# Kernel tuning notes

Hardware: AMD Instinct MI355X
Metric: run time of the kernel (lower is better)

Reference implementation:

```python
import jax, jax.numpy as jnp
import numpy as np

VOCAB = 256
EMB = 128
HID = 512
OUT = 256
B = 64
L = 1024


def setup_inputs() -> dict:
    key = jax.random.key(0)
    ks = jax.random.split(key, 6)
    x = jax.random.randint(ks[0], (B, L), 0, VOCAB, dtype=jnp.int32)
    hidden = jnp.zeros((B, HID), dtype=jnp.float32)
    embedding = jax.random.normal(ks[1], (VOCAB, EMB), dtype=jnp.float32)
    W_e = jax.random.normal(ks[2], (EMB, HID), dtype=jnp.float32) * 0.01
    W_h = jax.random.normal(ks[3], (HID, HID), dtype=jnp.float32) * 0.01
    b_h = jnp.zeros((1, HID), dtype=jnp.float32)
    W_o = jax.random.normal(ks[4], (HID, OUT), dtype=jnp.float32) * 0.01
    b_o = jnp.zeros((OUT,), dtype=jnp.float32)
    return {"x": x, "hidden": hidden, "embedding": embedding, "W_e": W_e,
            "W_h": W_h, "b_h": b_h, "W_o": W_o, "b_o": b_o}


def reference(x, hidden, embedding, W_e, W_h, b_h, W_o, b_o):
    # x: [b, l] int ids -> embed: [l, b, emb] (time-major for the scan)
    x_embed = embedding[x]                      # [b, l, emb]
    x_embed = jnp.swapaxes(x_embed, 0, 1)       # [l, b, emb]
    # Precompute input projection for all timesteps (same math, batched):
    hx_all = jnp.einsum('lbe,eh->lbh', x_embed, W_e)  # [l, b, hid]

    def step(h_prev, hx_t):
        h_t = jnp.tanh(hx_t + h_prev @ W_h + b_h)
        return h_t, h_t

    final_hidden, outputs = jax.lax.scan(step, hidden, hx_all)  # outputs: [l, b, hid]
    outputs = jnp.swapaxes(outputs, 0, 1)                        # [b, l, hid]
    logits = outputs @ W_o + b_o                                  # [b, l, out]
    return logits, final_hidden
```

## Files before the change

kernel.cpp:

```cpp
#include <hip/hip_runtime.h>

typedef float f32x4 __attribute__((ext_vector_type(4)));
typedef int   i32x4 __attribute__((ext_vector_type(4)));
typedef short s16x8 __attribute__((ext_vector_type(8)));

#define VOCAB 256
#define EMB   128
#define HID   512
#define OUT_D 256
#define BATCH 64
#define SEQ   1024

__device__ __forceinline__ unsigned short f2bf(float f) {
  unsigned u = __builtin_bit_cast(unsigned, f);
  u += 0x7fffu + ((u >> 16) & 1u);
  return (unsigned short)(u >> 16);
}

__global__ void k_e2(const float* __restrict__ emb, const float* __restrict__ We,
                     const float* __restrict__ bh, float* __restrict__ E2)
{
  __shared__ float el[EMB];
  const int v = blockIdx.x, c = threadIdx.x;
  if (c < EMB) el[c] = emb[v * EMB + c];
  __syncthreads();
  float s = bh[c];
  #pragma unroll
  for (int e = 0; e < EMB; ++e) s += el[e] * We[e * HID + c];
  E2[v * HID + c] = s;
}

__global__ void k_whfrag(const float* __restrict__ Wh, i32x4* __restrict__ WhF)
{
  const int g = blockIdx.x * 256 + threadIdx.x;
  const int lane = g & 63, frag = g >> 6;
  const int kt = frag & 7, nt = (frag >> 3) & 3, w = frag >> 5;
  const int col = (w << 6) + (nt << 4) + (lane & 15);
  const int kb  = (kt << 6) + ((lane >> 4) << 4);
  int wd[4];
  #pragma unroll
  for (int q = 0; q < 4; ++q) {
    int b[4];
    #pragma unroll
    for (int j = 0; j < 4; ++j) {
      float s = Wh[(kb + q * 4 + j) * HID + col] * 2048.f;
      s = fminf(fmaxf(s, -127.f), 127.f);
      b[j] = __float2int_rn(s) & 255;
    }
    wd[q] = b[0] | (b[1] << 8) | (b[2] << 16) | (b[3] << 24);
  }
  i32x4 v = {wd[0], wd[1], wd[2], wd[3]};
  WhF[g] = v;
}

__global__ void k_wot(const float* __restrict__ Wo, unsigned short* __restrict__ WoT)
{
  const int k = blockIdx.x;
  const int c = threadIdx.x;
  WoT[c * HID + k] = f2bf(Wo[k * OUT_D + c] * (1.0f / 127.0f));
}

__global__ __launch_bounds__(512, 2) void k_scan(
    const int* __restrict__ x, const float* __restrict__ h0,
    const float* __restrict__ E2, const i32x4* __restrict__ WhF,
    char* __restrict__ hist, float* __restrict__ fh)
{
  __shared__ __align__(16) char hbuf[2][HID];
  const int tid  = threadIdx.x;
  const int wv   = tid >> 6, lane = tid & 63;
  const int lrow = lane & 15, lhi = lane >> 4;
  const int row  = blockIdx.x;
  const int col  = (wv << 6) + (lhi << 4) + lrow;

  i32x4 bfr[4][8];
  #pragma unroll
  for (int nt = 0; nt < 4; ++nt)
    #pragma unroll
    for (int kt = 0; kt < 8; ++kt)
      bfr[nt][kt] = WhF[((((wv << 2) + nt) << 3) + kt) * 64 + lane];

  {
    float s = fminf(fmaxf(h0[(row << 9) + tid] * 127.f, -127.f), 127.f);
    hbuf[0][tid] = (char)__float2int_rn(s);
  }

  const int id0 = x[(row << 10) + 0];
  int idA = x[(row << 10) + 1], idB;
  float hxA = E2[(id0 << 9) + col], hxB;
  __syncthreads();

  const float inv = 1.f / (127.f * 2048.f);
  const float TC  = 2.8853900817779268f;

#define STEP(T, PH, HXU, HXP, IDU, IDL)                                       \
  {                                                                           \
    const int t_ = (T);                                                       \
           \
    i32x4 fv;                                                                 \
    if (tid < 32) fv = *(const i32x4*)(&hbuf[PH][tid << 4]);                  \
                 \
    HXP = E2[((IDU) << 9) + col];                                             \
                                               \
    IDL = x[(row << 10) + ((t_ + 2 > SEQ - 1) ? SEQ - 1 : t_ + 2)];           \
      \
    i32x4 acc[4] = {};                                                        \
    _Pragma("unroll") for (int kt = 0; kt < 8; ++kt) {                        \
      i32x4 a = *(const i32x4*)(&hbuf[PH][(kt << 6) + (lhi << 4)]);           \
      _Pragma("unroll") for (int nt = 0; nt < 4; ++nt)                        \
        acc[nt] = __builtin_amdgcn_mfma_i32_16x16x64_i8(a, bfr[nt][kt],       \
                                                        acc[nt], 0, 0, 0);    \
    }                                                                         \
                     \
    if (t_ > 0 && tid < 32)                                                   \
      __builtin_nontemporal_store(fv, (i32x4*)(hist +                         \
          (((size_t)(row << 10) + (t_ - 1)) << 10) + (tid << 4)));            \
      \
    int a01 = (lhi & 1) ? acc[1][0] : acc[0][0];                              \
    int a23 = (lhi & 1) ? acc[3][0] : acc[2][0];                              \
    int av  = (lhi & 2) ? a23 : a01;                                          \
                              \
    float z = fmaf((float)av, inv, HXU);                                      \
    float e = __builtin_amdgcn_exp2f(z * TC);                                 \
    float h = fmaf(-2.f, __builtin_amdgcn_rcpf(1.f + e), 1.f);                \
    hbuf[1 - (PH)][col] = (char)__float2int_rn(h * 127.f);                    \
    if (t_ == SEQ - 1) fh[(row << 9) + col] = h;                              \
    asm volatile("s_waitcnt lgkmcnt(0)" ::: "memory");                        \
    __builtin_amdgcn_sched_barrier(0);                                        \
    __builtin_amdgcn_s_barrier();                                             \
    __builtin_amdgcn_sched_barrier(0);                                        \
  }

  for (int T2 = 0; T2 < SEQ / 2; ++T2) {
    STEP(2 * T2,     0, hxA, hxB, idA, idB)
    STEP(2 * T2 + 1, 1, hxB, hxA, idB, idA)
  }
#undef STEP

  if (tid < 32) {
    i32x4 fv = *(const i32x4*)(&hbuf[0][tid << 4]);
    __builtin_nontemporal_store(fv, (i32x4*)(hist +
        (((size_t)(row << 10) + (SEQ - 1)) << 10) + (tid << 4)));
  }
}

__global__ __launch_bounds__(256) void k_logits(const char* __restrict__ hist,
                                                const unsigned short* __restrict__ WoT,
                                                const float* __restrict__ bo, float* out)
{
  __shared__ __align__(16) char As[64 * 1024];
  const int tid = threadIdx.x;
  const int m0 = blockIdx.x * 64;

  for (int i = tid; i < 1024; i += 256) {
    const int row = i >> 4, seg = i & 15;
    const char* src = hist + (size_t)(m0 + row) * 1024 + seg * 32;
    i32x4 w0 = *(const i32x4*)(src);
    i32x4 w1 = *(const i32x4*)(src + 16);
    unsigned od[16];
    #pragma unroll
    for (int d = 0; d < 8; ++d) {
      const unsigned dw = (unsigned)(d < 4 ? w0[d] : w1[d - 4]);
      const int q0 = (int)(signed char)(dw & 0xffu);
      const int q1 = (int)(signed char)((dw >> 8) & 0xffu);
      const int q2 = (int)(signed char)((dw >> 16) & 0xffu);
      const int q3 = (int)(signed char)(dw >> 24);
      const unsigned u0 = __builtin_bit_cast(unsigned, (float)q0);
      const unsigned u1 = __builtin_bit_cast(unsigned, (float)q1);
      const unsigned u2 = __builtin_bit_cast(unsigned, (float)q2);
      const unsigned u3 = __builtin_bit_cast(unsigned, (float)q3);
      od[2 * d]     = (u0 >> 16) | (u1 & 0xffff0000u);
      od[2 * d + 1] = (u2 >> 16) | (u3 & 0xffff0000u);
    }
    #pragma unroll
    for (int q = 0; q < 4; ++q) {
      i32x4 v = {(int)od[4 * q], (int)od[4 * q + 1],
                 (int)od[4 * q + 2], (int)od[4 * q + 3]};
      const int off = seg * 64 + q * 16;
      *(i32x4*)(&As[row * 1024 + (off ^ ((row & 7) << 4))]) = v;
    }
  }
  __syncthreads();

  const int wv = tid >> 6, lane = tid & 63, lrow = lane & 15, lhi = lane >> 4;
  const int cb = wv << 6;
  f32x4 acc[4][4] = {};
  #pragma unroll
  for (int kt = 0; kt < 16; ++kt) {
    s16x8 a[4], b[4];
    #pragma unroll
    for (int mt = 0; mt < 4; ++mt) {
      const int row = mt * 16 + lrow;
      a[mt] = *(const s16x8*)(&As[row * 1024 + ((kt * 64 + lhi * 16) ^ ((row & 7) << 4))]);
    }
    #pragma unroll
    for (int nt = 0; nt < 4; ++nt) {
      const int col = cb + nt * 16 + lrow;
      b[nt] = *(const s16x8*)((const char*)WoT + col * 1024 + kt * 64 + lhi * 16);
    }
    #pragma unroll
    for (int mt = 0; mt < 4; ++mt)
      #pragma unroll
      for (int nt = 0; nt < 4; ++nt)
        acc[mt][nt] = __builtin_amdgcn_mfma_f32_16x16x32_bf16(a[mt], b[nt], acc[mt][nt], 0, 0, 0);
  }
  #pragma unroll
  for (int nt = 0; nt < 4; ++nt) {
    const float bb = bo[cb + nt * 16 + lrow];
    #pragma unroll
    for (int mt = 0; mt < 4; ++mt)
      #pragma unroll
      for (int r = 0; r < 4; ++r)
        out[(size_t)(m0 + mt * 16 + lhi * 4 + r) * OUT_D + cb + nt * 16 + lrow] =
            acc[mt][nt][r] + bb;
  }
}

extern "C" void kernel_launch(void* const* d_in, const int* in_sizes, int n_in,
                              void* d_out, int out_size, void* d_ws, size_t ws_size,
                              hipStream_t stream)
{
  const int*   x   = (const int*)  d_in[0];
  const float* h0  = (const float*)d_in[1];
  const float* emb = (const float*)d_in[2];
  const float* We  = (const float*)d_in[3];
  const float* Wh  = (const float*)d_in[4];
  const float* bh  = (const float*)d_in[5];
  const float* Wo  = (const float*)d_in[6];
  const float* bo  = (const float*)d_in[7];
  float* out = (float*)d_out;
  char*  ws  = (char*)d_ws;

  float*          E2  = (float*)ws;
  i32x4*          WhF = (i32x4*)(ws + (512 << 10));
  unsigned short* WoT = (unsigned short*)(ws + (768 << 10));

  k_e2    <<<VOCAB, HID,   0, stream>>>(emb, We, bh, E2);
  k_whfrag<<<64,    256,   0, stream>>>(Wh, WhF);
  k_wot   <<<HID,   OUT_D, 0, stream>>>(Wo, WoT);

  k_scan  <<<BATCH, 512, 0, stream>>>(x, h0, E2, WhF,
                                      (char*)d_out,
                                      out + (size_t)BATCH * SEQ * OUT_D);
  k_logits<<<(BATCH * SEQ) / 64, 256, 0, stream>>>(
      (const char*)d_out, WoT, bo, out);
}
```

Baseline: 734.8 us.

## Split recurrent matvec between int8 MFMA and per-lane sdot4 over last K quarter

The recurrent h@W_h product is split along K. The first 384 rows stay on int8 MFMA with fewer fragments. The last 128 rows are computed per lane with sdot4 dot products against a new column-major int8 copy of W_h held in registers, and a new prep kernel builds that copy. The goal is to shorten the serial MFMA dependency chain on each timestep by overlapping it with VALU dot products, at the cost of extra LDS reads and register pressure.

New measurement: 726.5 us. No clear change (-1.1%).

```diff
diff --git a/kernel.cpp b/kernel.cpp
--- a/kernel.cpp
+++ b/kernel.cpp
@@ -34,8 +34,8 @@
 {
   const int g = blockIdx.x * 256 + threadIdx.x;
   const int lane = g & 63, frag = g >> 6;
-  const int kt = frag & 7, nt = (frag >> 3) & 3, w = frag >> 5;
-  const int col = (w << 6) + (nt << 4) + (lane & 15);
+  const int kt = frag & 7, ct = frag >> 3;
+  const int col = (ct << 4) + (lane & 15);
   const int kb  = (kt << 6) + ((lane >> 4) << 4);
   int wd[4];
   #pragma unroll
@@ -53,6 +53,21 @@
   WhF[g] = v;
 }
 
+__global__ void k_wv(const float* __restrict__ Wh, int* __restrict__ Wv)
+{
+  const int g = blockIdx.x * 256 + threadIdx.x;
+  const int col = g >> 5, d = g & 31;
+  const int k = 384 + d * 4;
+  int b[4];
+  #pragma unroll
+  for (int j = 0; j < 4; ++j) {
+    float s = Wh[(k + j) * HID + col] * 2048.f;
+    s = fminf(fmaxf(s, -127.f), 127.f);
+    b[j] = __float2int_rn(s) & 255;
+  }
+  Wv[(col << 5) + d] = b[0] | (b[1] << 8) | (b[2] << 16) | (b[3] << 24);
+}
+
 __global__ void k_wot(const float* __restrict__ Wo, unsigned short* __restrict__ WoT)
 {
   const int k = blockIdx.x;
@@ -63,6 +78,7 @@
 __global__ __launch_bounds__(512, 2) void k_scan(
     const int* __restrict__ x, const float* __restrict__ h0,
     const float* __restrict__ E2, const i32x4* __restrict__ WhF,
+    const int* __restrict__ Wv,
     char* __restrict__ hist, float* __restrict__ fh)
 {
   __shared__ __align__(16) char hbuf[2][HID];
@@ -72,12 +88,16 @@
   const int row  = blockIdx.x;
   const int col  = (wv << 6) + (lhi << 4) + lrow;
 
-  i32x4 bfr[4][8];
+  i32x4 bfr[4][6];
   #pragma unroll
   for (int nt = 0; nt < 4; ++nt)
     #pragma unroll
-    for (int kt = 0; kt < 8; ++kt)
+    for (int kt = 0; kt < 6; ++kt)
       bfr[nt][kt] = WhF[((((wv << 2) + nt) << 3) + kt) * 64 + lane];
+
+  int wvr[32];
+  #pragma unroll
+  for (int d = 0; d < 32; ++d) wvr[d] = Wv[(col << 5) + d];
 
   {
     float s = fminf(fmaxf(h0[(row << 9) + tid] * 127.f, -127.f), 127.f);
@@ -102,9 +122,18 @@
     HXP = E2[((IDU) << 9) + col];                                             \
                                                \
     IDL = x[(row << 10) + ((t_ + 2 > SEQ - 1) ? SEQ - 1 : t_ + 2)];           \
+         \
+    int dd = 0;                                                               \
+    _Pragma("unroll") for (int q = 0; q < 8; ++q) {                           \
+      i32x4 hq = *(const i32x4*)(&hbuf[PH][384 + (q << 4)]);                  \
+      dd = __builtin_amdgcn_sdot4(hq[0], wvr[4 * q + 0], dd, false);          \
+      dd = __builtin_amdgcn_sdot4(hq[1], wvr[4 * q + 1], dd, false);          \
+      dd = __builtin_amdgcn_sdot4(hq[2], wvr[4 * q + 2], dd, false);          \
+      dd = __builtin_amdgcn_sdot4(hq[3], wvr[4 * q + 3], dd, false);          \
+    }                                                                         \
       \
     i32x4 acc[4] = {};                                                        \
-    _Pragma("unroll") for (int kt = 0; kt < 8; ++kt) {                        \
+    _Pragma("unroll") for (int kt = 0; kt < 6; ++kt) {                        \
       i32x4 a = *(const i32x4*)(&hbuf[PH][(kt << 6) + (lhi << 4)]);           \
       _Pragma("unroll") for (int nt = 0; nt < 4; ++nt)                        \
         acc[nt] = __builtin_amdgcn_mfma_i32_16x16x64_i8(a, bfr[nt][kt],       \
@@ -118,8 +147,8 @@
     int a01 = (lhi & 1) ? acc[1][0] : acc[0][0];                              \
     int a23 = (lhi & 1) ? acc[3][0] : acc[2][0];                              \
     int av  = (lhi & 2) ? a23 : a01;                                          \
-                              \
-    float z = fmaf((float)av, inv, HXU);                                      \
+                       \
+    float z = fmaf((float)(av + dd), inv, HXU);                               \
     float e = __builtin_amdgcn_exp2f(z * TC);                                 \
     float h = fmaf(-2.f, __builtin_amdgcn_rcpf(1.f + e), 1.f);                \
     hbuf[1 - (PH)][col] = (char)__float2int_rn(h * 127.f);                    \
@@ -233,12 +262,14 @@
   float*          E2  = (float*)ws;
   i32x4*          WhF = (i32x4*)(ws + (512 << 10));
   unsigned short* WoT = (unsigned short*)(ws + (768 << 10));
+  int*            Wv  = (int*)(ws + (1024 << 10));
 
   k_e2    <<<VOCAB, HID,   0, stream>>>(emb, We, bh, E2);
   k_whfrag<<<64,    256,   0, stream>>>(Wh, WhF);
+  k_wv    <<<64,    256,   0, stream>>>(Wh, Wv);
   k_wot   <<<HID,   OUT_D, 0, stream>>>(Wo, WoT);
 
-  k_scan  <<<BATCH, 512, 0, stream>>>(x, h0, E2, WhF,
+  k_scan  <<<BATCH, 512, 0, stream>>>(x, h0, E2, WhF, Wv,
                                       (char*)d_out,
                                       out + (size_t)BATCH * SEQ * OUT_D);
   k_logits<<<(BATCH * SEQ) / 64, 256, 0, stream>>>(
```
